# Kernel tuning notes

Measured on AMD Instinct MI355X. Metric: run time of the kernel, lower is better.

The kernel has to match this reference:

```python
import jax, jax.numpy as jnp
import numpy as np

EPS = 1e-7


def squash(s):
    # safe norm over last axis, keepdims
    norm = jnp.sqrt(jnp.sum(jnp.square(s), axis=-1, keepdims=True) + EPS)
    norm_sq = jnp.square(norm)
    return norm_sq / (1.0 + norm_sq) / norm * s


def setup_inputs() -> dict:
    key = jax.random.key(0)
    k1, k2 = jax.random.split(key)
    B, IN_CAPS, IN_DIM = 64, 2048, 16
    N_CAPS, CAP_DIM = 64, 16
    x = jax.random.normal(k1, (B, IN_CAPS, IN_DIM), dtype=jnp.float32)
    # glorot-uniform-ish init for W
    limit = (6.0 / (IN_DIM + N_CAPS * CAP_DIM)) ** 0.5
    W = jax.random.uniform(k2, (IN_CAPS, IN_DIM, N_CAPS * CAP_DIM),
                           minval=-limit, maxval=limit, dtype=jnp.float32)
    bias = jnp.zeros((N_CAPS, CAP_DIM), dtype=jnp.float32)
    return {"x": x, "W": W, "bias": bias}


def reference(x, W, bias):
    B, in_caps, in_dim = x.shape
    n_caps, cap_dim = bias.shape
    r_iters = 3
    # projection: [B, in_caps, n_caps*cap_dim] -> [B, in_caps, n_caps, cap_dim]
    u_hat = jnp.einsum('bij,ijk->bik', x, W).reshape(B, in_caps, n_caps, cap_dim)
    b = jnp.zeros((B, in_caps, n_caps, 1), dtype=u_hat.dtype)
    v = None
    for r in range(r_iters):
        c = jax.nn.softmax(b, axis=2)                       # route over class caps
        s = jnp.sum(u_hat * c, axis=1, keepdims=True)       # [B, 1, n_caps, cap_dim]
        s = s + bias
        v = squash(s)
        if r < r_iters - 1:
            agreement = jnp.sum(u_hat * v, axis=-1, keepdims=True)
            b = b + agreement
    return jnp.squeeze(v, axis=1)                           # [B, n_caps, cap_dim]
```

## Files before the change

### kernel.cpp

```cpp
#include <hip/hip_runtime.h>
#include <hip/hip_bf16.h>
#include <hip/hip_fp16.h>
#include <cstdio>

#define B_  64
#define I_  2048
#define J_  16
#define N_  64
#define D_  16
#define K_  1024

using short8 = __attribute__((ext_vector_type(8))) short;
using f32x16 = __attribute__((ext_vector_type(16))) float;

#if __has_builtin(__builtin_amdgcn_cvt_pk_u8_f32)
#define CVTPK_U8(f, sel, old) (unsigned)__builtin_amdgcn_cvt_pk_u8_f32((f), (sel), (old))
#else
__device__ __forceinline__ unsigned cvtpk_u8_sw(float f, unsigned sel, unsigned old) {
  unsigned b = (unsigned)(int)f & 0xffu;
  unsigned sh = sel * 8u;
  return (old & ~(0xffu << sh)) | (b << sh);
}
#define CVTPK_U8(f, sel, old) cvtpk_u8_sw((f), (sel), (old))
#endif

__device__ __forceinline__ short8 pack_bf16x8(float a0, float a1, float a2, float a3,
                                              float a4, float a5, float a6, float a7) {
  __hip_bfloat162 p0 = __float22bfloat162_rn(float2{a0, a1});
  __hip_bfloat162 p1 = __float22bfloat162_rn(float2{a2, a3});
  __hip_bfloat162 p2 = __float22bfloat162_rn(float2{a4, a5});
  __hip_bfloat162 p3 = __float22bfloat162_rn(float2{a6, a7});
  union { unsigned u[4]; short8 s; } cv;
  cv.u[0] = *(unsigned*)&p0; cv.u[1] = *(unsigned*)&p1;
  cv.u[2] = *(unsigned*)&p2; cv.u[3] = *(unsigned*)&p3;
  return cv.s;
}

__global__ __launch_bounds__(256) void project_k(const float* __restrict__ x,
                                                 const float* __restrict__ W,
                                                 unsigned char* __restrict__ uh,
                                                 unsigned short* __restrict__ sc) {
  const int i  = blockIdx.x;
  const int t  = threadIdx.x;
  const int l  = t & 63;
  const int wv = t >> 6;
  const int h  = l >> 5;
  const int lr = l & 31;

  __shared__ unsigned short lds_w[256 * 20];
  __shared__ float          lds_x[64 * 20];
  __shared__ unsigned int   out_lds[64 * 64];
  __shared__ unsigned short sc_lds[64 * 20];

  {
    int b = t >> 2, q = t & 3;
    float4 v = ((const float4*)(x + ((size_t)b * I_ + i) * J_))[q];
    *(float4*)&lds_x[b * 20 + q * 4] = v;
  }
  __syncthreads();

  short8 xfrag;
  {
    int b = (wv & 1) * 32 + lr;
    const float* xp = &lds_x[b * 20 + h * 8];
    float4 f0 = *(const float4*)xp;
    float4 f1 = *(const float4*)(xp + 4);
    xfrag = pack_bf16x8(f0.x, f0.y, f0.z, f0.w, f1.x, f1.y, f1.z, f1.w);
  }

  const int b  = (wv & 1) * 32 + lr;
  const unsigned sw = (unsigned)((b & 7) << 2);
  const int kt_base = (wv >> 1) * 4;

  for (int ph = 0; ph < 4; ++ph) {
    {
      const float* wp = W + (size_t)i * (J_ * K_) + ph * 256;
      const int j0 = (t & 3) * 4;
      const int kg = t >> 2;
      float4 r0 = *(const float4*)(wp + (size_t)(j0 + 0) * K_ + kg * 4);
      float4 r1 = *(const float4*)(wp + (size_t)(j0 + 1) * K_ + kg * 4);
      float4 r2 = *(const float4*)(wp + (size_t)(j0 + 2) * K_ + kg * 4);
      float4 r3 = *(const float4*)(wp + (size_t)(j0 + 3) * K_ + kg * 4);
      const float* p0 = (const float*)&r0;
      const float* p1 = (const float*)&r1;
      const float* p2 = (const float*)&r2;
      const float* p3 = (const float*)&r3;
#pragma unroll
      for (int kk = 0; kk < 4; ++kk) {
        __hip_bfloat162 pA = __float22bfloat162_rn(float2{p0[kk], p1[kk]});
        __hip_bfloat162 pB = __float22bfloat162_rn(float2{p2[kk], p3[kk]});
        uint2 u; u.x = *(unsigned*)&pA; u.y = *(unsigned*)&pB;
        *(uint2*)&lds_w[(kg * 4 + kk) * 20 + j0] = u;
      }
    }
    __syncthreads();

#pragma unroll
    for (int kk = 0; kk < 4; ++kk) {
      const int kt = kt_base + kk;
      const unsigned short* ap = &lds_w[(kt * 32 + lr) * 20 + h * 8];
      union { uint2 u2[2]; short8 s; } cv;
      cv.u2[0] = *(const uint2*)ap;
      cv.u2[1] = *(const uint2*)(ap + 4);
      f32x16 acc = {0.f, 0.f, 0.f, 0.f, 0.f, 0.f, 0.f, 0.f,
                    0.f, 0.f, 0.f, 0.f, 0.f, 0.f, 0.f, 0.f};
      acc = __builtin_amdgcn_mfma_f32_32x32x16_bf16(cv.s, xfrag, acc, 0, 0, 0);

#define QCAP(C8, CS) do {                                                       \
      float ax = fabsf(acc[(C8) + 0]);                                          \
      ax = fmaxf(ax, fabsf(acc[(C8) + 1]));                                     \
      ax = fmaxf(ax, fabsf(acc[(C8) + 2]));                                     \
      ax = fmaxf(ax, fabsf(acc[(C8) + 3]));                                     \
      ax = fmaxf(ax, fabsf(acc[(C8) + 4]));                                     \
      ax = fmaxf(ax, fabsf(acc[(C8) + 5]));                                     \
      ax = fmaxf(ax, fabsf(acc[(C8) + 6]));                                     \
      ax = fmaxf(ax, fabsf(acc[(C8) + 7]));                                     \
      ax = fmaxf(ax, __shfl_xor(ax, 32));                                       \
      float inv = __fdividef(127.0f, fmaxf(ax, 1e-30f));                        \
      unsigned pk0 = CVTPK_U8(rintf(fmaf(acc[(C8) + 0], inv, 128.f)), 0u, 0u);  \
      pk0 = CVTPK_U8(rintf(fmaf(acc[(C8) + 1], inv, 128.f)), 1u, pk0);          \
      pk0 = CVTPK_U8(rintf(fmaf(acc[(C8) + 2], inv, 128.f)), 2u, pk0);          \
      pk0 = CVTPK_U8(rintf(fmaf(acc[(C8) + 3], inv, 128.f)), 3u, pk0);          \
      unsigned pk1 = CVTPK_U8(rintf(fmaf(acc[(C8) + 4], inv, 128.f)), 0u, 0u);  \
      pk1 = CVTPK_U8(rintf(fmaf(acc[(C8) + 5], inv, 128.f)), 1u, pk1);          \
      pk1 = CVTPK_U8(rintf(fmaf(acc[(C8) + 6], inv, 128.f)), 2u, pk1);          \
      pk1 = CVTPK_U8(rintf(fmaf(acc[(C8) + 7], inv, 128.f)), 3u, pk1);          \
      const int ibase = kt * 8 + (CS) * 4;                                      \
      out_lds[b * 64 + ((unsigned)(ibase + h)     ^ sw)] = pk0;                 \
      out_lds[b * 64 + ((unsigned)(ibase + 2 + h) ^ sw)] = pk1;                 \
      if (h == 0)                                                               \
        sc_lds[b * 20 + kt * 2 + (CS)] =                                        \
            __half_as_ushort(__float2half_rn(ax * (1.0f / 127.0f)));            \
    } while (0)

      QCAP(0, 0);
      QCAP(8, 1);
#undef QCAP
    }
    __syncthreads();

    {
      const int c = t & 15;
#pragma unroll
      for (int it = 0; it < 4; ++it) {
        int bf = (t >> 4) + it * 16;
        uint4 v = *(const uint4*)&out_lds[bf * 64 + (((unsigned)(c * 4)) ^ ((unsigned)((bf & 7) << 2)))];
        *(uint4*)(uh + (size_t)bf * I_ * K_ + (size_t)i * K_ + ph * 256 + c * 16) = v;
      }
      int b2 = t >> 2, n4 = (t & 3) * 4;
      uint2 sv = *(const uint2*)&sc_lds[b2 * 20 + n4];
      *(uint2*)(sc + (size_t)b2 * I_ * N_ + (size_t)i * N_ + ph * 16 + n4) = sv;
    }
    __syncthreads();
  }
}

template <int MODE>
__global__ __launch_bounds__(256, 4) void route_k(const unsigned char* __restrict__ uh,
                                                  const unsigned short* __restrict__ sc,
                                                  const float* __restrict__ sa,
                                                  const float* __restrict__ sb,
                                                  const float* __restrict__ bias,
                                                  float* __restrict__ s_out) {
  const int t    = threadIdx.x;
  const int lane = t & 63;
  const int wv   = t >> 6;
  const int b    = blockIdx.x >> 4;
  const int iw   = ((blockIdx.x & 15) << 2) + wv;
  const int i0   = iw * 32;

  float vsum[16];
  float voff = 0.f;
  if (MODE >= 1) {
    float bs[16];
#pragma unroll
    for (int q = 0; q < 4; ++q) {
      float4 bb4 = *(const float4*)&bias[lane * 16 + q * 4];
      bs[q*4+0] = bb4.x; bs[q*4+1] = bb4.y; bs[q*4+2] = bb4.z; bs[q*4+3] = bb4.w;
    }
    {
      float va[16], nn = 0.f;
#pragma unroll
      for (int q = 0; q < 4; ++q) {
        float4 tmp = *(const float4*)&sa[(size_t)b * K_ + lane * 16 + q * 4];
        va[q*4+0] = tmp.x + bs[q*4+0]; va[q*4+1] = tmp.y + bs[q*4+1];
        va[q*4+2] = tmp.z + bs[q*4+2]; va[q*4+3] = tmp.w + bs[q*4+3];
      }
#pragma unroll
      for (int d = 0; d < 16; ++d) nn += va[d] * va[d];
      float n2 = nn + 1e-7f;
      float f = sqrtf(n2) / (1.0f + n2);
#pragma unroll
      for (int d = 0; d < 16; ++d) vsum[d] = va[d] * f;
    }
    if (MODE == 2) {
      float vb[16], nn = 0.f;
#pragma unroll
      for (int q = 0; q < 4; ++q) {
        float4 tmp = *(const float4*)&sb[(size_t)b * K_ + lane * 16 + q * 4];
        vb[q*4+0] = tmp.x + bs[q*4+0]; vb[q*4+1] = tmp.y + bs[q*4+1];
        vb[q*4+2] = tmp.z + bs[q*4+2]; vb[q*4+3] = tmp.w + bs[q*4+3];
      }
#pragma unroll
      for (int d = 0; d < 16; ++d) nn += vb[d] * vb[d];
      float n2 = nn + 1e-7f;
      float f = sqrtf(n2) / (1.0f + n2);
#pragma unroll
      for (int d = 0; d < 16; ++d) vsum[d] += vb[d] * f;
    }
    float tv = 0.f;
#pragma unroll
    for (int d = 0; d < 16; ++d) tv += vsum[d];
    voff = 128.0f * tv;
  }

  constexpr int IPW = 32;
  constexpr int PF  = 4;

  const unsigned char*  base = uh + (size_t)b * I_ * K_ + lane * 16;
  const unsigned short* scb  = sc + (size_t)b * I_ * N_ + lane;

  uint4 dbuf[PF];
  unsigned short hbuf[PF];
#pragma unroll
  for (int p = 0; p < PF; ++p) {
    int ip = (i0 + p) & (I_ - 1);
    dbuf[p] = *(const uint4*)(base + (size_t)ip * K_);
    hbuf[p] = scb[(size_t)ip * N_];
  }

  float s_loc[16];
#pragma unroll
  for (int d = 0; d < 16; ++d) s_loc[d] = 0.f;
  float csum = 0.f;

  for (int ii = 0; ii < IPW; ii += PF) {
#pragma unroll
    for (int p = 0; p < PF; ++p) {
      float scale = __half2float(__ushort_as_half(hbuf[p]));
      float u[16];
      {
        unsigned wd;
        wd = dbuf[p].x;
        u[0]  = (float)(wd & 0xffu);         u[1]  = (float)((wd >> 8) & 0xffu);
        u[2]  = (float)((wd >> 16) & 0xffu); u[3]  = (float)(wd >> 24);
        wd = dbuf[p].y;
        u[4]  = (float)(wd & 0xffu);         u[5]  = (float)((wd >> 8) & 0xffu);
        u[6]  = (float)((wd >> 16) & 0xffu); u[7]  = (float)(wd >> 24);
        wd = dbuf[p].z;
        u[8]  = (float)(wd & 0xffu);         u[9]  = (float)((wd >> 8) & 0xffu);
        u[10] = (float)((wd >> 16) & 0xffu); u[11] = (float)(wd >> 24);
        wd = dbuf[p].w;
        u[12] = (float)(wd & 0xffu);         u[13] = (float)((wd >> 8) & 0xffu);
        u[14] = (float)((wd >> 16) & 0xffu); u[15] = (float)(wd >> 24);
      }

      int ip = (i0 + ii + p + PF) & (I_ - 1);
      dbuf[p] = *(const uint4*)(base + (size_t)ip * K_);
      hbuf[p] = scb[(size_t)ip * N_];

      if (MODE == 0) {
#pragma unroll
        for (int d = 0; d < 16; ++d) s_loc[d] = fmaf(scale, u[d], s_loc[d]);
        csum += scale;
      } else {
        float dot = 0.f;
#pragma unroll
        for (int d = 0; d < 16; ++d) dot = fmaf(u[d], vsum[d], dot);
        float bl = scale * (dot - voff);
        float m = bl;
        m = fmaxf(m, __shfl_xor(m, 1));
        m = fmaxf(m, __shfl_xor(m, 2));
        m = fmaxf(m, __shfl_xor(m, 4));
        m = fmaxf(m, __shfl_xor(m, 8));
        m = fmaxf(m, __shfl_xor(m, 16));
        m = fmaxf(m, __shfl_xor(m, 32));
        float e = __expf(bl - m);
        float ss = e;
        ss += __shfl_xor(ss, 1);
        ss += __shfl_xor(ss, 2);
        ss += __shfl_xor(ss, 4);
        ss += __shfl_xor(ss, 8);
        ss += __shfl_xor(ss, 16);
        ss += __shfl_xor(ss, 32);
        float cs = __fdividef(e, ss) * scale;
#pragma unroll
        for (int d = 0; d < 16; ++d) s_loc[d] = fmaf(cs, u[d], s_loc[d]);
        csum += cs;
      }
    }
  }

#pragma unroll
  for (int d = 0; d < 16; ++d) s_loc[d] -= 128.0f * csum;
  if (MODE == 0) {
#pragma unroll
    for (int d = 0; d < 16; ++d) s_loc[d] *= (1.0f / 64.0f);
  }

  __shared__ float sred[4][64 * 17];
#pragma unroll
  for (int d = 0; d < 16; ++d) sred[wv][lane * 17 + d] = s_loc[d];
  __syncthreads();
#pragma unroll
  for (int e = 0; e < 4; ++e) {
    int idx = t * 4 + e;
    int n = idx >> 4, d = idx & 15;
    float val = sred[0][n*17+d] + sred[1][n*17+d] + sred[2][n*17+d] + sred[3][n*17+d];
    atomicAdd(&s_out[(size_t)b * K_ + idx], val);
  }
}

__global__ __launch_bounds__(256) void squash_k(const float* __restrict__ s_in,
                                                const float* __restrict__ bias,
                                                float* __restrict__ v_out) {
  const int b = blockIdx.x, t = threadIdx.x, k0 = t * 4;
  float4 s = *(const float4*)&s_in[b * K_ + k0];
  float4 bb = *(const float4*)&bias[k0];
  s.x += bb.x; s.y += bb.y; s.z += bb.z; s.w += bb.w;
  float p = s.x * s.x + s.y * s.y + s.z * s.z + s.w * s.w;
  p += __shfl_xor(p, 1);
  p += __shfl_xor(p, 2);
  float n2 = p + 1e-7f;
  float nrm = sqrtf(n2);
  float f = nrm / (1.0f + n2);
  float4 o = {s.x * f, s.y * f, s.z * f, s.w * f};
  *(float4*)&v_out[b * K_ + k0] = o;
}

extern "C" void kernel_launch(void* const* d_in, const int* in_sizes, int n_in,
                              void* d_out, int out_size, void* d_ws, size_t ws_size,
                              hipStream_t stream) {
  const float* x    = (const float*)d_in[0];
  const float* W    = (const float*)d_in[1];
  const float* bias = (const float*)d_in[2];
  float* out = (float*)d_out;

  char* ws = (char*)d_ws;
  size_t off = 0;
  unsigned char*  uh = (unsigned char*)(ws + off);  off += (size_t)B_ * I_ * K_;
  unsigned short* sc = (unsigned short*)(ws + off); off += (size_t)B_ * I_ * N_ * 2;
  float* s0 = (float*)(ws + off); off += (size_t)B_ * K_ * 4;
  float* s1 = (float*)(ws + off); off += (size_t)B_ * K_ * 4;
  float* s2 = (float*)(ws + off); off += (size_t)B_ * K_ * 4;

  if (ws_size < off)
    fprintf(stderr, "ClassCapsule: ws_size=%zu < needed=%zu — expect corruption\n", ws_size, off);

  (void)hipMemsetAsync(s0, 0, (size_t)3 * B_ * K_ * 4, stream);

  project_k<<<dim3(I_), dim3(256), 0, stream>>>(x, W, uh, sc);

  route_k<0><<<dim3(1024), dim3(256), 0, stream>>>(uh, sc, nullptr, nullptr, bias, s0);
  route_k<1><<<dim3(1024), dim3(256), 0, stream>>>(uh, sc, s0, nullptr, bias, s1);
  route_k<2><<<dim3(1024), dim3(256), 0, stream>>>(uh, sc, s0, s1, bias, s2);
  squash_k<<<dim3(B_), dim3(256), 0, stream>>>(s2, bias, out);
}
```

Measured before the change: 166.8 us.

## Split projection blocks across output phases, load W fragments directly, fold memset into kernel

```diff
diff --git a/kernel.cpp b/kernel.cpp
--- a/kernel.cpp
+++ b/kernel.cpp
@@ -36,75 +36,50 @@
   return cv.s;
 }
 
-__global__ __launch_bounds__(256) void project_k(const float* __restrict__ x,
-                                                 const float* __restrict__ W,
-                                                 unsigned char* __restrict__ uh,
-                                                 unsigned short* __restrict__ sc) {
-  const int i  = blockIdx.x;
+__global__ __launch_bounds__(256, 5) void project_k(const float* __restrict__ x,
+                                                    const float* __restrict__ W,
+                                                    unsigned char* __restrict__ uh,
+                                                    unsigned short* __restrict__ sc,
+                                                    float* __restrict__ s_zero) {
+  const int i  = blockIdx.x >> 2;
+  const int ph = blockIdx.x & 3;
   const int t  = threadIdx.x;
   const int l  = t & 63;
   const int wv = t >> 6;
   const int h  = l >> 5;
   const int lr = l & 31;
 
-  __shared__ unsigned short lds_w[256 * 20];
-  __shared__ float          lds_x[64 * 20];
-  __shared__ unsigned int   out_lds[64 * 64];
+  __shared__ unsigned       out_lds[64 * 65];
   __shared__ unsigned short sc_lds[64 * 20];
 
-  {
-    int b = t >> 2, q = t & 3;
-    float4 v = ((const float4*)(x + ((size_t)b * I_ + i) * J_))[q];
-    *(float4*)&lds_x[b * 20 + q * 4] = v;
-  }
-  __syncthreads();
-
-  short8 xfrag;
-  {
-    int b = (wv & 1) * 32 + lr;
-    const float* xp = &lds_x[b * 20 + h * 8];
+  if (blockIdx.x < 768) s_zero[blockIdx.x * 256 + t] = 0.f;
+
+  short8 xfrag[2];
+#pragma unroll
+  for (int bt = 0; bt < 2; ++bt) {
+    const float* xp = x + ((size_t)(bt * 32 + lr) * I_ + i) * J_ + h * 8;
     float4 f0 = *(const float4*)xp;
     float4 f1 = *(const float4*)(xp + 4);
-    xfrag = pack_bf16x8(f0.x, f0.y, f0.z, f0.w, f1.x, f1.y, f1.z, f1.w);
-  }
-
-  const int b  = (wv & 1) * 32 + lr;
-  const unsigned sw = (unsigned)((b & 7) << 2);
-  const int kt_base = (wv >> 1) * 4;
-
-  for (int ph = 0; ph < 4; ++ph) {
-    {
-      const float* wp = W + (size_t)i * (J_ * K_) + ph * 256;
-      const int j0 = (t & 3) * 4;
-      const int kg = t >> 2;
-      float4 r0 = *(const float4*)(wp + (size_t)(j0 + 0) * K_ + kg * 4);
-      float4 r1 = *(const float4*)(wp + (size_t)(j0 + 1) * K_ + kg * 4);
-      float4 r2 = *(const float4*)(wp + (size_t)(j0 + 2) * K_ + kg * 4);
-      float4 r3 = *(const float4*)(wp + (size_t)(j0 + 3) * K_ + kg * 4);
-      const float* p0 = (const float*)&r0;
-      const float* p1 = (const float*)&r1;
-      const float* p2 = (const float*)&r2;
-      const float* p3 = (const float*)&r3;
-#pragma unroll
-      for (int kk = 0; kk < 4; ++kk) {
-        __hip_bfloat162 pA = __float22bfloat162_rn(float2{p0[kk], p1[kk]});
-        __hip_bfloat162 pB = __float22bfloat162_rn(float2{p2[kk], p3[kk]});
-        uint2 u; u.x = *(unsigned*)&pA; u.y = *(unsigned*)&pB;
-        *(uint2*)&lds_w[(kg * 4 + kk) * 20 + j0] = u;
-      }
-    }
-    __syncthreads();
-
-#pragma unroll
-    for (int kk = 0; kk < 4; ++kk) {
-      const int kt = kt_base + kk;
-      const unsigned short* ap = &lds_w[(kt * 32 + lr) * 20 + h * 8];
-      union { uint2 u2[2]; short8 s; } cv;
-      cv.u2[0] = *(const uint2*)ap;
-      cv.u2[1] = *(const uint2*)(ap + 4);
+    xfrag[bt] = pack_bf16x8(f0.x, f0.y, f0.z, f0.w, f1.x, f1.y, f1.z, f1.w);
+  }
+
+  const float* wbase = W + (size_t)i * (J_ * K_) + ph * 256;
+
+#pragma unroll
+  for (int kx = 0; kx < 2; ++kx) {
+    const int kt = wv * 2 + kx;
+    float wf[8];
+#pragma unroll
+    for (int e = 0; e < 8; ++e)
+      wf[e] = wbase[(size_t)(h * 8 + e) * K_ + kt * 32 + lr];
+    short8 afrag = pack_bf16x8(wf[0], wf[1], wf[2], wf[3], wf[4], wf[5], wf[6], wf[7]);
+
+#pragma unroll
+    for (int bt = 0; bt < 2; ++bt) {
       f32x16 acc = {0.f, 0.f, 0.f, 0.f, 0.f, 0.f, 0.f, 0.f,
                     0.f, 0.f, 0.f, 0.f, 0.f, 0.f, 0.f, 0.f};
-      acc = __builtin_amdgcn_mfma_f32_32x32x16_bf16(cv.s, xfrag, acc, 0, 0, 0);
+      acc = __builtin_amdgcn_mfma_f32_32x32x16_bf16(afrag, xfrag[bt], acc, 0, 0, 0);
+      const int b = bt * 32 + lr;
 
 #define QCAP(C8, CS) do {                                                       \
       float ax = fabsf(acc[(C8) + 0]);                                          \
@@ -126,8 +101,8 @@
       pk1 = CVTPK_U8(rintf(fmaf(acc[(C8) + 6], inv, 128.f)), 2u, pk1);          \
       pk1 = CVTPK_U8(rintf(fmaf(acc[(C8) + 7], inv, 128.f)), 3u, pk1);          \
       const int ibase = kt * 8 + (CS) * 4;                                      \
-      out_lds[b * 64 + ((unsigned)(ibase + h)     ^ sw)] = pk0;                 \
-      out_lds[b * 64 + ((unsigned)(ibase + 2 + h) ^ sw)] = pk1;                 \
+      out_lds[b * 65 + ibase + h]     = pk0;                                    \
+      out_lds[b * 65 + ibase + 2 + h] = pk1;                                    \
       if (h == 0)                                                               \
         sc_lds[b * 20 + kt * 2 + (CS)] =                                        \
             __half_as_ushort(__float2half_rn(ax * (1.0f / 127.0f)));            \
@@ -137,21 +112,22 @@
       QCAP(8, 1);
 #undef QCAP
     }
-    __syncthreads();
-
-    {
-      const int c = t & 15;
-#pragma unroll
-      for (int it = 0; it < 4; ++it) {
-        int bf = (t >> 4) + it * 16;
-        uint4 v = *(const uint4*)&out_lds[bf * 64 + (((unsigned)(c * 4)) ^ ((unsigned)((bf & 7) << 2)))];
-        *(uint4*)(uh + (size_t)bf * I_ * K_ + (size_t)i * K_ + ph * 256 + c * 16) = v;
-      }
-      int b2 = t >> 2, n4 = (t & 3) * 4;
-      uint2 sv = *(const uint2*)&sc_lds[b2 * 20 + n4];
-      *(uint2*)(sc + (size_t)b2 * I_ * N_ + (size_t)i * N_ + ph * 16 + n4) = sv;
-    }
-    __syncthreads();
+  }
+  __syncthreads();
+
+  {
+    const int c = t & 15;
+#pragma unroll
+    for (int it = 0; it < 4; ++it) {
+      int bf = (t >> 4) + it * 16;
+      const unsigned* rp = &out_lds[bf * 65 + c * 4];
+      uint4 v;
+      v.x = rp[0]; v.y = rp[1]; v.z = rp[2]; v.w = rp[3];
+      *(uint4*)(uh + (size_t)bf * I_ * K_ + (size_t)i * K_ + ph * 256 + c * 16) = v;
+    }
+    int b2 = t >> 2, n4 = (t & 3) * 4;
+    uint2 sv = *(const uint2*)&sc_lds[b2 * 20 + n4];
+    *(uint2*)(sc + (size_t)b2 * I_ * N_ + (size_t)i * N_ + ph * 16 + n4) = sv;
   }
 }
 
@@ -347,9 +323,7 @@
   if (ws_size < off)
     fprintf(stderr, "ClassCapsule: ws_size=%zu < needed=%zu — expect corruption\n", ws_size, off);
 
-  (void)hipMemsetAsync(s0, 0, (size_t)3 * B_ * K_ * 4, stream);
-
-  project_k<<<dim3(I_), dim3(256), 0, stream>>>(x, W, uh, sc);
+  project_k<<<dim3(I_ * 4), dim3(256), 0, stream>>>(x, W, uh, sc, s0);
 
   route_k<0><<<dim3(1024), dim3(256), 0, stream>>>(uh, sc, nullptr, nullptr, bias, s0);
   route_k<1><<<dim3(1024), dim3(256), 0, stream>>>(uh, sc, s0, nullptr, bias, s1);
```

Measured after the change: 171.2 us. +2.6%, slower.
